# Kernel tuning notes

Measured on AMD Instinct MI355X. Metric: run time of the kernel, lower is better.

Reference implementation:

```python
import jax, jax.numpy as jnp
import numpy as np

EPS = 1e-5  # torch LayerNorm default


def _ln(x, g, b):
    m = x.mean(-1, keepdims=True)
    v = ((x - m) ** 2).mean(-1, keepdims=True)
    return (x - m) / jnp.sqrt(v + EPS) * g + b


def setup_inputs() -> dict:
    B, T, D, H, L = 4, 2048, 512, 8, 2
    key = jax.random.key(0)
    ks = jax.random.split(key, 16)
    w = lambda k, shp, fan: jax.random.normal(k, shp, jnp.float32) * (fan ** -0.5)
    return {
        "x_vid": jax.random.normal(ks[0], (B, T, D), jnp.float32),
        "x_aud": jax.random.normal(ks[1], (B, T, D), jnp.float32),
        "vid_kpm": jax.random.bernoulli(ks[2], 0.1, (B, T)),
        "aud_kpm": jax.random.bernoulli(ks[3], 0.1, (B, T)),
        "Wq_vid": w(ks[4], (L, D, D), D),
        "Wk_aud_for_vid": w(ks[5], (L, D, D), D),
        "Wq_aud": w(ks[6], (L, D, D), D),
        "Wk_vid_for_aud": w(ks[7], (L, D, D), D),
        "vg_W1": w(ks[8], (L, 2 * H, H), H),
        "vg_b1": jnp.zeros((L, 2 * H), jnp.float32),
        "vg_W2": w(ks[9], (L, 1, 2 * H), 2 * H),
        "vg_b2": jnp.zeros((L, 1), jnp.float32),
        "ag_W1": w(ks[10], (L, 2 * H, H), H),
        "ag_b1": jnp.zeros((L, 2 * H), jnp.float32),
        "ag_W2": w(ks[11], (L, 1, 2 * H), 2 * H),
        "ag_b2": jnp.zeros((L, 1), jnp.float32),
        "vid_ln_g": jnp.ones((L, D), jnp.float32),
        "vid_ln_b": jnp.zeros((L, D), jnp.float32),
        "aud_ln_g": jnp.ones((L, D), jnp.float32),
        "aud_ln_b": jnp.zeros((L, D), jnp.float32),
    }


def reference(x_vid, x_aud, vid_kpm, aud_kpm,
              Wq_vid, Wk_aud_for_vid, Wq_aud, Wk_vid_for_aud,
              vg_W1, vg_b1, vg_W2, vg_b2,
              ag_W1, ag_b1, ag_W2, ag_b2,
              vid_ln_g, vid_ln_b, aud_ln_g, aud_ln_b):
    B, T, D = x_vid.shape
    L = Wq_vid.shape[0]
    H = vg_W1.shape[-1]
    dh = D // H
    scale = dh ** -0.5

    def heads(x):  # (B,T,D) -> (B,H,T,dh)
        return x.reshape(B, T, H, dh).transpose(0, 2, 1, 3)

    # mask-derived constants
    aud_valid = jnp.clip((~aud_kpm).sum(-1).astype(jnp.float32), 1.0)[:, None, None]  # (B,1,1)
    vid_valid = jnp.clip((~vid_kpm).sum(-1).astype(jnp.float32), 1.0)[:, None, None]
    aud_all = aud_kpm.all(-1)  # (B,)
    vid_all = vid_kpm.all(-1)

    def gate_mlp(rel, W1, b1, W2, b2):  # rel: (B,T,H) -> (B,T,1)
        h1 = jax.nn.relu(jnp.einsum('bth,eh->bte', rel, W1) + b1)
        return jax.nn.sigmoid(jnp.einsum('bte,oe->bto', h1, W2) + b2)

    for i in range(L):
        # --- vid gated by attention to aud (NOTE: source applies vid_norms to BOTH) ---
        vid_n = _ln(x_vid, vid_ln_g[i], vid_ln_b[i])
        aud_n = _ln(x_aud, vid_ln_g[i], vid_ln_b[i])
        q = heads(jnp.einsum('btd,od->bto', vid_n, Wq_vid[i]))
        k = heads(jnp.einsum('btd,od->bto', aud_n, Wk_aud_for_vid[i]))
        logits = jnp.einsum('bhtd,bhsd->bhts', q, k) * scale  # (B,H,T,T)
        logits = jnp.where(aud_kpm[:, None, None, :], 0.0, logits)
        rel = logits.sum(-1) / aud_valid           # (B,H,T)
        rel = rel.transpose(0, 2, 1)               # (B,T,H)
        gate_v = gate_mlp(rel, vg_W1[i], vg_b1[i], vg_W2[i], vg_b2[i])
        gate_v = jnp.where(aud_all[:, None, None], 0.0, gate_v)
        x_vid = x_vid + x_vid * gate_v             # dropout is identity at eval

        # --- aud gated by attention to (updated) vid; source applies aud_norms to BOTH ---
        aud_n = _ln(x_aud, aud_ln_g[i], aud_ln_b[i])
        vid_n = _ln(x_vid, aud_ln_g[i], aud_ln_b[i])
        q = heads(jnp.einsum('btd,od->bto', aud_n, Wq_aud[i]))
        k = heads(jnp.einsum('btd,od->bto', vid_n, Wk_vid_for_aud[i]))
        logits = jnp.einsum('bhtd,bhsd->bhts', q, k) * scale
        logits = jnp.where(vid_kpm[:, None, None, :], 0.0, logits)
        rel = (logits.sum(-1) / vid_valid).transpose(0, 2, 1)
        gate_a = gate_mlp(rel, ag_W1[i], ag_b1[i], ag_W2[i], ag_b2[i])
        gate_a = jnp.where(vid_all[:, None, None], 0.0, gate_a)
        x_aud = x_aud + x_aud * gate_a

    return (x_vid, x_aud)
```

## Files before the change

### kernel.cpp

```cpp
#include <hip/hip_runtime.h>
#include <math.h>

#define BB 4
#define TT 2048
#define DD 512
#define HH 8
#define EPS 1e-5f
#define SCALE 0.125f
#define WW ((size_t)DD * DD)


__device__ __forceinline__ float wred(float s) {
#pragma unroll
  for (int o = 32; o > 0; o >>= 1) s += __shfl_xor(s, o);
  return s;
}

__device__ __forceinline__ void ldf(const float* p, int lane, float f[8]) {
  float4 a = *reinterpret_cast<const float4*>(p + lane * 4);
  float4 c = *reinterpret_cast<const float4*>(p + 256 + lane * 4);
  f[0]=a.x; f[1]=a.y; f[2]=a.z; f[3]=a.w;
  f[4]=c.x; f[5]=c.y; f[6]=c.z; f[7]=c.w;
}

__global__ __launch_bounds__(256) void sums_kernel(
    const float* __restrict__ xv, const float* __restrict__ xa,
    const int* __restrict__ vkpm, const int* __restrict__ akpm,
    float* __restrict__ partial)
{
  const int blk  = blockIdx.x;
  const int s    = blk >> 8;
  const int b    = (blk >> 6) & 3;
  const int tile = blk & 63;
  const int wave = threadIdx.x >> 6, lane = threadIdx.x & 63;
  const float* x  = s ? xa : xv;
  const int* kpm  = s ? akpm : vkpm;
  const int row0  = b * TT + tile * 32 + wave * 8;

  __shared__ float lds[4][DD];

  float acc[8] = {0.f,0.f,0.f,0.f,0.f,0.f,0.f,0.f};
  for (int r = 0; r < 8; ++r) {
    const int row = row0 + r;
    float v[8]; ldf(x + (size_t)row * DD, lane, v);
    float s1 = 0.f, s2 = 0.f;
#pragma unroll
    for (int k = 0; k < 8; ++k) { s1 += v[k]; s2 += v[k]*v[k]; }
    s1 = wred(s1); s2 = wred(s2);
    const float mean = s1 * (1.f / (float)DD);
    const float var  = s2 * (1.f / (float)DD) - mean * mean;
    const float rstd = rsqrtf(var + EPS);
    if (kpm[row] == 0) {
#pragma unroll
      for (int k = 0; k < 8; ++k) acc[k] += (v[k] - mean) * rstd;
    }
  }
#pragma unroll
  for (int k = 0; k < 4; ++k) {
    lds[wave][lane*4+k]       = acc[k];
    lds[wave][256+lane*4+k]   = acc[4+k];
  }
  __syncthreads();
  const int tid = threadIdx.x;
  float s0 = lds[0][tid] + lds[1][tid] + lds[2][tid] + lds[3][tid];
  float s1 = lds[0][tid+256] + lds[1][tid+256] + lds[2][tid+256] + lds[3][tid+256];
  float* p = partial + ((size_t)(s*4 + b) * 64 + tile) * DD;
  p[tid]       = s0;
  p[tid + 256] = s1;
}

__global__ __launch_bounds__(256) void mphase2_kernel(
    const float* __restrict__ partial,
    const int* __restrict__ vkpm, const int* __restrict__ akpm,
    const float* __restrict__ Wq_v, const float* __restrict__ Wk_av,
    const float* __restrict__ Wq_a, const float* __restrict__ Wk_va,
    const float* __restrict__ vid_g, const float* __restrict__ vid_b,
    const float* __restrict__ aud_g, const float* __restrict__ aud_b,
    float* __restrict__ mp,
    float* __restrict__ cv,
    float* __restrict__ smv,
    float* __restrict__ fs)
{
  const int blk = blockIdx.x;
  const int p = blk >> 5, b = (blk >> 3) & 3, h = blk & 7;
  const int layer = p >> 1;
  const int isA = ((p & 1) == 0);
  const int tid = threadIdx.x, wave = tid >> 6, lane = tid & 63;

  __shared__ float4 red[256];
  __shared__ float nsum_s[DD];
  __shared__ float ksl[64];
  __shared__ float csh[4];
  __shared__ float cs2[4], ss2[4];

  const int ksb = (isA ? 1 : 0) * 4 + b;

  {
    const int half = tid >> 7;
    const int i    = tid & 127;
    const float* pp = partial + ((size_t)ksb * 64 + half * 32) * DD + i * 4;
    float4 acc = make_float4(0.f, 0.f, 0.f, 0.f);
#pragma unroll 8
    for (int t = 0; t < 32; ++t) {
      float4 u = *reinterpret_cast<const float4*>(pp + (size_t)t * DD);
      acc.x += u.x; acc.y += u.y; acc.z += u.z; acc.w += u.w;
    }
    red[tid] = acc;
  }

  const int* mk = isA ? akpm : vkpm;
  {
    int cnt = 0;
#pragma unroll
    for (int q = 0; q < 8; ++q) cnt += (mk[b * TT + q * 256 + tid] == 0) ? 1 : 0;
    float fc = wred((float)cnt);
    if (lane == 0) csh[wave] = fc;
  }
  __syncthreads();
  if (tid < 128) {
    float4 a0 = red[tid], a1 = red[tid + 128];
    *reinterpret_cast<float4*>(&nsum_s[tid * 4]) =
        make_float4(a0.x + a1.x, a0.y + a1.y, a0.z + a1.z, a0.w + a1.w);
  }
  __syncthreads();

  const float vc   = csh[0] + csh[1] + csh[2] + csh[3];
  const float fac  = SCALE / fmaxf(vc, 1.f);
  const float cntf = vc;
  if (layer == 0 && h == 0 && tid == 0) {
    fs[ksb * 4 + 0] = fac;
    fs[ksb * 4 + 1] = (vc > 0.f) ? 1.f : 0.f;
    fs[ksb * 4 + 2] = vc;
  }

  const float* g  = (isA ? vid_g : aud_g) + (size_t)layer * DD;
  const float* be = (isA ? vid_b : aud_b) + (size_t)layer * DD;
  const float* Wk = (isA ? Wk_av : Wk_va) + (size_t)layer * WW;
  const float* Wq = (isA ? Wq_v  : Wq_a ) + (size_t)layer * WW;

  float gv[8], bv[8], sv[8], nl[8];
  ldf(g, lane, gv); ldf(be, lane, bv);
  {
    float4 a = *reinterpret_cast<const float4*>(&nsum_s[lane * 4]);
    float4 c = *reinterpret_cast<const float4*>(&nsum_s[256 + lane * 4]);
    sv[0]=a.x; sv[1]=a.y; sv[2]=a.z; sv[3]=a.w;
    sv[4]=c.x; sv[5]=c.y; sv[6]=c.z; sv[7]=c.w;
  }
#pragma unroll
  for (int k = 0; k < 8; ++k) nl[k] = sv[k]*gv[k] + cntf*bv[k];

#pragma unroll 4
  for (int jj = 0; jj < 16; ++jj) {
    const int j = wave * 16 + jj;
    float w[8]; ldf(Wk + (size_t)(h*64 + j) * DD, lane, w);
    float sdot = w[0]*nl[0]+w[1]*nl[1]+w[2]*nl[2]+w[3]*nl[3]
               + w[4]*nl[4]+w[5]*nl[5]+w[6]*nl[6]+w[7]*nl[7];
    sdot = wred(sdot);
    if (lane == 0) ksl[j] = sdot * fac;
  }
  __syncthreads();

  float a0 = 0.f, a1 = 0.f;
  const float* base = Wq + (size_t)(h*64) * DD;
#pragma unroll 16
  for (int j = 0; j < 64; ++j) {
    const float kk = ksl[j];
    a0 += base[(size_t)j*DD + tid]       * kk;
    a1 += base[(size_t)j*DD + tid + 256] * kk;
  }

  const float gq0 = g[tid], gq1 = g[tid + 256];
  const float bq0 = be[tid], bq1 = be[tid + 256];
  const float mp0 = a0 * gq0, mp1 = a1 * gq1;
  float* mo = mp + (((size_t)p*4 + b)*8 + h) * DD;
  mo[tid]       = mp0;
  mo[tid + 256] = mp1;

  float cp = a0*bq0 + a1*bq1;
  float sp = mp0 + mp1;
  cp = wred(cp); sp = wred(sp);
  if (lane == 0) { cs2[wave] = cp; ss2[wave] = sp; }
  __syncthreads();
  if (tid == 0) {
    const int idx = ((p*4 + b)*8 + h);
    cv[idx]  = cs2[0]+cs2[1]+cs2[2]+cs2[3];
    smv[idx] = ss2[0]+ss2[1]+ss2[2]+ss2[3];
  }
}

__global__ __launch_bounds__(256) void final_kernel(
    const float* __restrict__ xv_in, const float* __restrict__ xa_in,
    const float* __restrict__ mp, const float* __restrict__ cv,
    const float* __restrict__ smv, const float* __restrict__ fs,
    const float* __restrict__ vg_W1, const float* __restrict__ vg_b1,
    const float* __restrict__ vg_W2, const float* __restrict__ vg_b2,
    const float* __restrict__ ag_W1, const float* __restrict__ ag_b1,
    const float* __restrict__ ag_W2, const float* __restrict__ ag_b2,
    float* __restrict__ out_v, float* __restrict__ out_a)
{
  const int blk = blockIdx.x;
  const int s = blk >> 10, b = (blk >> 8) & 3, tile = blk & 255;
  const int tid = threadIdx.x, lane = tid & 63;
  const int wave = tid >> 6;
  const float* x = s ? xa_in : xv_in;
  float* out     = s ? out_a : out_v;
  const int row0 = b * TT + tile * 8 + wave * 2;

  __shared__ float mlp[2][161];
  {
    const float* W1p = s ? ag_W1 : vg_W1;
    const float* b1p = s ? ag_b1 : vg_b1;
    const float* W2p = s ? ag_W2 : vg_W2;
    const float* b2p = s ? ag_b2 : vg_b2;
    if (tid < 128)       { mlp[0][tid] = W1p[tid];       mlp[1][tid] = W1p[128 + tid]; }
    else if (tid < 144)  { mlp[0][tid] = b1p[tid - 128]; mlp[1][tid] = b1p[tid - 112]; }
    else if (tid < 160)  { mlp[0][tid] = W2p[tid - 144]; mlp[1][tid] = W2p[tid - 128]; }
    else if (tid == 160) { mlp[0][160] = b2p[0];         mlp[1][160] = b2p[1]; }
  }
  __syncthreads();

  const float flag = fs[(((s ? 0 : 1) * 4) + b) * 4 + 1];

  float v[2][8];
  float myMean = 0.f, myRstd = 1.f;
#pragma unroll
  for (int r = 0; r < 2; ++r) {
    ldf(x + (size_t)(row0 + r) * DD, lane, v[r]);
    float s1 = 0.f, s2 = 0.f;
#pragma unroll
    for (int k = 0; k < 8; ++k) { s1 += v[r][k]; s2 += v[r][k]*v[r][k]; }
    s1 = wred(s1); s2 = wred(s2);
    const float mean = s1 * (1.f / (float)DD);
    const float rstd = rsqrtf(s2 * (1.f / (float)DD) - mean*mean + EPS);
    if ((lane & 1) == r) { myMean = mean; myRstd = rstd; }
  }

  float a[32];
  const float* mpb0 = mp + ((size_t)(s*4 + b) * 8) * DD;
  const float* mpb1 = mp + ((size_t)((2+s)*4 + b) * 8) * DD;
#pragma unroll
  for (int l = 0; l < 2; ++l) {
    const float* mb_ = l ? mpb1 : mpb0;
#pragma unroll
    for (int h = 0; h < HH; ++h) {
      float w[8]; ldf(mb_ + (size_t)h * DD, lane, w);
      const int j = l*8 + h;
#pragma unroll
      for (int r = 0; r < 2; ++r) {
        a[r*16 + j] = v[r][0]*w[0] + v[r][1]*w[1] + v[r][2]*w[2] + v[r][3]*w[3]
                    + v[r][4]*w[4] + v[r][5]*w[5] + v[r][6]*w[6] + v[r][7]*w[7];
      }
    }
  }

#pragma unroll
  for (int k = 0; k < 5; ++k) {
    const int bit = (lane >> k) & 1;
#pragma unroll
    for (int m = 0; m < (32 >> (k + 1)); ++m) {
      const float keep = bit ? a[2*m+1] : a[2*m];
      const float send = bit ? a[2*m]   : a[2*m+1];
      a[m] = keep + __shfl_xor(send, 1 << k);
    }
  }
  const float dotv = a[0] + __shfl_xor(a[0], 32);

  const int gr = lane & 1, gl = (lane >> 1) & 1;
  float q[8];
#pragma unroll
  for (int h = 0; h < HH; ++h) q[h] = __shfl(dotv, gr*16 + gl*8 + h);

  float gpart = 1.f;
  if (lane < 4) {
    const int l = lane >> 1;
    const int p = l*2 + s;
    const float* cb  = cv  + ((size_t)p*4 + b) * 8;
    const float* sbv = smv + ((size_t)p*4 + b) * 8;
    float rel[8];
#pragma unroll
    for (int h = 0; h < HH; ++h)
      rel[h] = myRstd * (q[h] - myMean * sbv[h]) + cb[h];
    float z = mlp[l][160];
#pragma unroll
    for (int e = 0; e < 16; ++e) {
      float h1 = mlp[l][128 + e];
#pragma unroll
      for (int h = 0; h < HH; ++h) h1 += rel[h] * mlp[l][e*8 + h];
      z += fmaxf(h1, 0.f) * mlp[l][144 + e];
    }
    gpart = 1.f + flag * (1.f / (1.f + expf(-z)));
  }

#pragma unroll
  for (int r = 0; r < 2; ++r) {
    const float sc = __shfl(gpart, r) * __shfl(gpart, 2 + r);
    float* orow = out + (size_t)(row0 + r) * DD;
    *reinterpret_cast<float4*>(orow + lane*4) =
        make_float4(v[r][0]*sc, v[r][1]*sc, v[r][2]*sc, v[r][3]*sc);
    *reinterpret_cast<float4*>(orow + 256 + lane*4) =
        make_float4(v[r][4]*sc, v[r][5]*sc, v[r][6]*sc, v[r][7]*sc);
  }
}

extern "C" void kernel_launch(void* const* d_in, const int* in_sizes, int n_in,
                              void* d_out, int out_size, void* d_ws, size_t ws_size,
                              hipStream_t stream) {
  const float* x_vid = (const float*)d_in[0];
  const float* x_aud = (const float*)d_in[1];
  const int* vid_kpm = (const int*)d_in[2];
  const int* aud_kpm = (const int*)d_in[3];
  const float* Wq_vid         = (const float*)d_in[4];
  const float* Wk_aud_for_vid = (const float*)d_in[5];
  const float* Wq_aud         = (const float*)d_in[6];
  const float* Wk_vid_for_aud = (const float*)d_in[7];
  const float* vg_W1 = (const float*)d_in[8];
  const float* vg_b1 = (const float*)d_in[9];
  const float* vg_W2 = (const float*)d_in[10];
  const float* vg_b2 = (const float*)d_in[11];
  const float* ag_W1 = (const float*)d_in[12];
  const float* ag_b1 = (const float*)d_in[13];
  const float* ag_W2 = (const float*)d_in[14];
  const float* ag_b2 = (const float*)d_in[15];
  const float* vid_ln_g = (const float*)d_in[16];
  const float* vid_ln_b = (const float*)d_in[17];
  const float* aud_ln_g = (const float*)d_in[18];
  const float* aud_ln_b = (const float*)d_in[19];

  const size_t BTD = (size_t)BB * TT * DD;
  float* out_v = (float*)d_out;
  float* out_a = out_v + BTD;

  float* partial = (float*)d_ws;
  float* fs      = partial + (size_t)8 * 64 * DD;
  float* mpw     = fs + 32;
  float* cvw     = mpw + (size_t)4 * 4 * 8 * DD;
  float* smw     = cvw + 128;

  sums_kernel<<<512, 256, 0, stream>>>(x_vid, x_aud, vid_kpm, aud_kpm, partial);
  mphase2_kernel<<<128, 256, 0, stream>>>(
      partial, vid_kpm, aud_kpm,
      Wq_vid, Wk_aud_for_vid, Wq_aud, Wk_vid_for_aud,
      vid_ln_g, vid_ln_b, aud_ln_g, aud_ln_b, mpw, cvw, smw, fs);
  final_kernel<<<2048, 256, 0, stream>>>(
      x_vid, x_aud, mpw, cvw, smw, fs,
      vg_W1, vg_b1, vg_W2, vg_b2, ag_W1, ag_b1, ag_W2, ag_b2,
      out_v, out_a);
}
```

Baseline: 49.22 us.

## Stage per-head projection vectors in LDS and process four rows per wave

The final kernel now handles 16 rows per block (4 per wave) and launches half as many blocks. The 16 projection vectors are loaded cooperatively into shared memory once per block, instead of each wave reading them from global/L2, and the row loads are issued before the barrier so they overlap the staging. The cv/smv constants also move into shared memory. The cost is 32KB of LDS per block and a larger register array (64 accumulators, plus a 6-stage shuffle reduction), which may lower occupancy.

```diff
diff --git a/kernel.cpp b/kernel.cpp
--- a/kernel.cpp
+++ b/kernel.cpp
@@ -199,87 +199,97 @@
     float* __restrict__ out_v, float* __restrict__ out_a)
 {
   const int blk = blockIdx.x;
-  const int s = blk >> 10, b = (blk >> 8) & 3, tile = blk & 255;
+  const int s = blk >> 9, b = (blk >> 7) & 3, tile = blk & 127;
   const int tid = threadIdx.x, lane = tid & 63;
   const int wave = tid >> 6;
   const float* x = s ? xa_in : xv_in;
   float* out     = s ? out_a : out_v;
-  const int row0 = b * TT + tile * 8 + wave * 2;
-
+  const int row0 = b * TT + tile * 16 + wave * 4;
+
+  __shared__ float mplds[16][DD];
   __shared__ float mlp[2][161];
+  __shared__ float cs[16], ss[16];
+
+  float v[4][8];
+  float myMean = 0.f, myRstd = 1.f;
+#pragma unroll
+  for (int r = 0; r < 4; ++r) {
+    ldf(x + (size_t)(row0 + r) * DD, lane, v[r]);
+    float s1 = 0.f, s2 = 0.f;
+#pragma unroll
+    for (int k = 0; k < 8; ++k) { s1 += v[r][k]; s2 += v[r][k]*v[r][k]; }
+    s1 = wred(s1); s2 = wred(s2);
+    const float mean = s1 * (1.f / (float)DD);
+    const float rstd = rsqrtf(s2 * (1.f / (float)DD) - mean*mean + EPS);
+    if ((lane & 3) == r) { myMean = mean; myRstd = rstd; }
+  }
+
   {
+    const float* mpb0 = mp + ((size_t)(s*4 + b) * 8) * DD;
+    const float* mpb1 = mp + ((size_t)((2+s)*4 + b) * 8) * DD;
+#pragma unroll
+    for (int i = tid; i < 2048; i += 256) {
+      const int j = i >> 7, pos = i & 127;
+      const float* src = (j < 8) ? (mpb0 + (size_t)j * DD) : (mpb1 + (size_t)(j-8) * DD);
+      *reinterpret_cast<float4*>(&mplds[j][pos * 4]) =
+          *reinterpret_cast<const float4*>(src + pos * 4);
+    }
+  }
+  if (tid < 16) {
+    const int l = tid >> 3, h = tid & 7;
+    const int p = l*2 + s;
+    cs[tid] = cv [((size_t)p*4 + b) * 8 + h];
+    ss[tid] = smv[((size_t)p*4 + b) * 8 + h];
+  } else if (tid >= 32 && tid < 193) {
+    const int t = tid - 32;
     const float* W1p = s ? ag_W1 : vg_W1;
     const float* b1p = s ? ag_b1 : vg_b1;
     const float* W2p = s ? ag_W2 : vg_W2;
     const float* b2p = s ? ag_b2 : vg_b2;
-    if (tid < 128)       { mlp[0][tid] = W1p[tid];       mlp[1][tid] = W1p[128 + tid]; }
-    else if (tid < 144)  { mlp[0][tid] = b1p[tid - 128]; mlp[1][tid] = b1p[tid - 112]; }
-    else if (tid < 160)  { mlp[0][tid] = W2p[tid - 144]; mlp[1][tid] = W2p[tid - 128]; }
-    else if (tid == 160) { mlp[0][160] = b2p[0];         mlp[1][160] = b2p[1]; }
+    if (t < 128)       { mlp[0][t] = W1p[t];       mlp[1][t] = W1p[128 + t]; }
+    else if (t < 144)  { mlp[0][t] = b1p[t - 128]; mlp[1][t] = b1p[t - 112]; }
+    else if (t < 160)  { mlp[0][t] = W2p[t - 144]; mlp[1][t] = W2p[t - 128]; }
+    else               { mlp[0][160] = b2p[0];     mlp[1][160] = b2p[1]; }
   }
   __syncthreads();
 
   const float flag = fs[(((s ? 0 : 1) * 4) + b) * 4 + 1];
 
-  float v[2][8];
-  float myMean = 0.f, myRstd = 1.f;
-#pragma unroll
-  for (int r = 0; r < 2; ++r) {
-    ldf(x + (size_t)(row0 + r) * DD, lane, v[r]);
-    float s1 = 0.f, s2 = 0.f;
-#pragma unroll
-    for (int k = 0; k < 8; ++k) { s1 += v[r][k]; s2 += v[r][k]*v[r][k]; }
-    s1 = wred(s1); s2 = wred(s2);
-    const float mean = s1 * (1.f / (float)DD);
-    const float rstd = rsqrtf(s2 * (1.f / (float)DD) - mean*mean + EPS);
-    if ((lane & 1) == r) { myMean = mean; myRstd = rstd; }
-  }
-
-  float a[32];
-  const float* mpb0 = mp + ((size_t)(s*4 + b) * 8) * DD;
-  const float* mpb1 = mp + ((size_t)((2+s)*4 + b) * 8) * DD;
-#pragma unroll
-  for (int l = 0; l < 2; ++l) {
-    const float* mb_ = l ? mpb1 : mpb0;
-#pragma unroll
-    for (int h = 0; h < HH; ++h) {
-      float w[8]; ldf(mb_ + (size_t)h * DD, lane, w);
-      const int j = l*8 + h;
-#pragma unroll
-      for (int r = 0; r < 2; ++r) {
-        a[r*16 + j] = v[r][0]*w[0] + v[r][1]*w[1] + v[r][2]*w[2] + v[r][3]*w[3]
-                    + v[r][4]*w[4] + v[r][5]*w[5] + v[r][6]*w[6] + v[r][7]*w[7];
-      }
-    }
-  }
-
-#pragma unroll
-  for (int k = 0; k < 5; ++k) {
+  float a[64];
+#pragma unroll
+  for (int j = 0; j < 16; ++j) {
+    float4 w0 = *reinterpret_cast<const float4*>(&mplds[j][lane * 4]);
+    float4 w1 = *reinterpret_cast<const float4*>(&mplds[j][256 + lane * 4]);
+#pragma unroll
+    for (int r = 0; r < 4; ++r) {
+      a[r*16 + j] = v[r][0]*w0.x + v[r][1]*w0.y + v[r][2]*w0.z + v[r][3]*w0.w
+                  + v[r][4]*w1.x + v[r][5]*w1.y + v[r][6]*w1.z + v[r][7]*w1.w;
+    }
+  }
+
+#pragma unroll
+  for (int k = 0; k < 6; ++k) {
     const int bit = (lane >> k) & 1;
 #pragma unroll
-    for (int m = 0; m < (32 >> (k + 1)); ++m) {
+    for (int m = 0; m < (64 >> (k + 1)); ++m) {
       const float keep = bit ? a[2*m+1] : a[2*m];
       const float send = bit ? a[2*m]   : a[2*m+1];
       a[m] = keep + __shfl_xor(send, 1 << k);
     }
   }
-  const float dotv = a[0] + __shfl_xor(a[0], 32);
-
-  const int gr = lane & 1, gl = (lane >> 1) & 1;
+
+  const int gr = lane & 3, gl = (lane >> 2) & 1;
   float q[8];
 #pragma unroll
-  for (int h = 0; h < HH; ++h) q[h] = __shfl(dotv, gr*16 + gl*8 + h);
+  for (int h = 0; h < HH; ++h) q[h] = __shfl(a[0], gr*16 + gl*8 + h);
 
   float gpart = 1.f;
-  if (lane < 4) {
-    const int l = lane >> 1;
-    const int p = l*2 + s;
-    const float* cb  = cv  + ((size_t)p*4 + b) * 8;
-    const float* sbv = smv + ((size_t)p*4 + b) * 8;
+  if (lane < 8) {
+    const int l = lane >> 2;
     float rel[8];
 #pragma unroll
     for (int h = 0; h < HH; ++h)
-      rel[h] = myRstd * (q[h] - myMean * sbv[h]) + cb[h];
+      rel[h] = myRstd * (q[h] - myMean * ss[l*8 + h]) + cs[l*8 + h];
     float z = mlp[l][160];
 #pragma unroll
     for (int e = 0; e < 16; ++e) {
@@ -292,8 +302,8 @@
   }
 
 #pragma unroll
-  for (int r = 0; r < 2; ++r) {
-    const float sc = __shfl(gpart, r) * __shfl(gpart, 2 + r);
+  for (int r = 0; r < 4; ++r) {
+    const float sc = __shfl(gpart, r) * __shfl(gpart, 4 + r);
     float* orow = out + (size_t)(row0 + r) * DD;
     *reinterpret_cast<float4*>(orow + lane*4) =
         make_float4(v[r][0]*sc, v[r][1]*sc, v[r][2]*sc, v[r][3]*sc);
@@ -341,7 +351,7 @@
       partial, vid_kpm, aud_kpm,
       Wq_vid, Wk_aud_for_vid, Wq_aud, Wk_vid_for_aud,
       vid_ln_g, vid_ln_b, aud_ln_g, aud_ln_b, mpw, cvw, smw, fs);
-  final_kernel<<<2048, 256, 0, stream>>>(
+  final_kernel<<<1024, 256, 0, stream>>>(
       x_vid, x_aud, mpw, cvw, smw, fs,
       vg_W1, vg_b1, vg_W2, vg_b2, ag_W1, ag_b1, ag_W2, ag_b2,
       out_v, out_a);
```

Result: slower. 51.40 us (+4.4%).
